# Kernel optimization log

Measured on AMD Instinct MI355X. Metric: run time of the kernel, lower is better.

## Reference

```python
import jax, jax.numpy as jnp
import numpy as np

N, E, F_IN, HEADS, OUT_PER_HEAD = 50000, 1600000, 128, 4, 32
NEG_SLOPE = 0.2  # LeakyReLU slope used by standard GATConv


def setup_inputs() -> dict:
    key = jax.random.key(0)
    ks = jax.random.split(key, 7)
    x = jax.random.normal(ks[0], (N, F_IN), dtype=jnp.float32)
    edge_src = jax.random.randint(ks[1], (E,), 0, N, dtype=jnp.int64)
    edge_dst = jax.random.randint(ks[2], (E,), 0, N, dtype=jnp.int64)
    W = jax.random.normal(ks[3], (F_IN, HEADS * OUT_PER_HEAD), dtype=jnp.float32) / np.float32(np.sqrt(F_IN))
    a_src = jax.random.normal(ks[4], (HEADS, OUT_PER_HEAD), dtype=jnp.float32) * 0.1
    a_dst = jax.random.normal(ks[5], (HEADS, OUT_PER_HEAD), dtype=jnp.float32) * 0.1
    bias = jnp.zeros((HEADS * OUT_PER_HEAD,), dtype=jnp.float32)
    return {"x": x, "W": W, "a_src": a_src, "a_dst": a_dst, "bias": bias,
            "edge_src": edge_src, "edge_dst": edge_dst}


def reference(x, W, a_src, a_dst, bias, edge_src, edge_dst):
    # GATConv with concat=True over a static edge list (the faithful
    # static-shape form of tf.where(adj>0.5) -> gather -> GAT -> scatter).
    n = x.shape[0]
    H, D = a_src.shape
    h = (x @ W).reshape(n, H, D)                      # [N,H,D] projected features
    # per-node attention logits for source / destination roles
    e_s = jnp.einsum('nhd,hd->nh', h, a_src)          # [N,H]
    e_d = jnp.einsum('nhd,hd->nh', h, a_dst)          # [N,H]
    # per-edge logits with LeakyReLU
    e = jax.nn.leaky_relu(e_s[edge_src] + e_d[edge_dst], NEG_SLOPE)  # [E,H]
    # numerically stable softmax over incoming edges of each destination node
    m = jax.ops.segment_max(e, edge_dst, num_segments=n)             # [N,H]
    m = jnp.where(jnp.isfinite(m), m, 0.0)
    alpha = jnp.exp(e - m[edge_dst])                                 # [E,H]
    denom = jax.ops.segment_sum(alpha, edge_dst, num_segments=n)     # [N,H]
    alpha = alpha / jnp.where(denom > 0, denom, 1.0)[edge_dst]
    # weighted aggregation of source features onto destinations
    msgs = alpha[:, :, None] * h[edge_src]                           # [E,H,D]
    out = jax.ops.segment_sum(msgs, edge_dst, num_segments=n)        # [N,H,D]
    return out.reshape(n, H * D) + bias
```

## Files before the change

### kernel.cpp

```cpp
#include <hip/hip_runtime.h>
#include <math.h>

#define NEG_SLOPE 0.2f
#define NB1 256
#define XROW 136
#define BSHIFT 5
#define BNODES 32
#define CAP 2048

typedef __attribute__((ext_vector_type(8))) short short8;
typedef __attribute__((ext_vector_type(4))) float floatx4;

__device__ __forceinline__ unsigned short f2bf(float f) {
    unsigned int u = __float_as_uint(f);
    u += 0x7fffu + ((u >> 16) & 1u);
    return (unsigned short)(u >> 16);
}
__device__ __forceinline__ float bf2f(unsigned short b) {
    return __uint_as_float(((unsigned int)b) << 16);
}
__device__ __forceinline__ float u2fl(unsigned int u) {
    return __uint_as_float(u << 16);
}
__device__ __forceinline__ float u2fh(unsigned int u) {
    return __uint_as_float(u & 0xffff0000u);
}

__device__ __forceinline__ void fma8(float* a, int o, float wt, const uint4& hv) {
    a[o + 0] = fmaf(wt, u2fl(hv.x), a[o + 0]);
    a[o + 1] = fmaf(wt, u2fh(hv.x), a[o + 1]);
    a[o + 2] = fmaf(wt, u2fl(hv.y), a[o + 2]);
    a[o + 3] = fmaf(wt, u2fh(hv.y), a[o + 3]);
    a[o + 4] = fmaf(wt, u2fl(hv.z), a[o + 4]);
    a[o + 5] = fmaf(wt, u2fh(hv.z), a[o + 5]);
    a[o + 6] = fmaf(wt, u2fl(hv.w), a[o + 6]);
    a[o + 7] = fmaf(wt, u2fh(hv.w), a[o + 7]);
}

__global__ __launch_bounds__(256) void prep_w_kernel(
    const float* __restrict__ W, unsigned short* __restrict__ WThi,
    unsigned short* __restrict__ WTlo, int* __restrict__ gcur, int nbuck)
{
    const int idx = blockIdx.x * 256 + threadIdx.x;
    const int j = idx >> 7, k = idx & 127;
    const float w = W[k * 128 + j];
    const unsigned short hi = f2bf(w);
    const unsigned short lo = f2bf(w - bf2f(hi));
    WThi[idx] = hi;
    WTlo[idx] = lo;
    if (idx < nbuck) gcur[idx] = idx * CAP;
}

__global__ __launch_bounds__(256) void mfma_gemm_kernel(
    const float* __restrict__ x, const unsigned short* __restrict__ WThi,
    const unsigned short* __restrict__ WTlo, const float* __restrict__ a_src,
    const float* __restrict__ a_dst, unsigned short* __restrict__ hb,
    float* __restrict__ es, float* __restrict__ ed, int n)
{
    __shared__ unsigned short Xhi[32 * XROW];
    __shared__ unsigned short Xlo[32 * XROW];
    const int t = threadIdx.x;
    const int wv = t >> 6, lane = t & 63;
    const int l16 = lane & 15, quad = lane >> 4;
    const int node_base = blockIdx.x * 32;

    short8 bh[4][2], bl[4][2];
    #pragma unroll
    for (int c = 0; c < 4; ++c) {
        #pragma unroll
        for (int u = 0; u < 2; ++u) {
            const int j = (wv * 2 + u) * 16 + l16;
            const int ko = c * 32 + quad * 8;
            bh[c][u] = *(const short8*)&WThi[j * 128 + ko];
            bl[c][u] = *(const short8*)&WTlo[j * 128 + ko];
        }
    }

    for (int i = t; i < 1024; i += 256) {
        const int nd = i >> 5;
        const int k4 = i & 31;
        float4 xv = make_float4(0.f, 0.f, 0.f, 0.f);
        if (node_base + nd < n)
            xv = ((const float4*)(x + (size_t)(node_base + nd) * 128))[k4];
        const unsigned short h0 = f2bf(xv.x), h1 = f2bf(xv.y),
                             h2 = f2bf(xv.z), h3 = f2bf(xv.w);
        const unsigned short l0 = f2bf(xv.x - bf2f(h0)), l1 = f2bf(xv.y - bf2f(h1)),
                             l2 = f2bf(xv.z - bf2f(h2)), l3 = f2bf(xv.w - bf2f(h3));
        *(ushort4*)&Xhi[nd * XROW + k4 * 4] = make_ushort4(h0, h1, h2, h3);
        *(ushort4*)&Xlo[nd * XROW + k4 * 4] = make_ushort4(l0, l1, l2, l3);
    }
    __syncthreads();

    floatx4 acc[2][2] = {};
    #pragma unroll
    for (int c = 0; c < 4; ++c) {
        const int ko = c * 32 + quad * 8;
        short8 ah[2], al[2];
        #pragma unroll
        for (int r = 0; r < 2; ++r) {
            ah[r] = *(const short8*)&Xhi[(r * 16 + l16) * XROW + ko];
            al[r] = *(const short8*)&Xlo[(r * 16 + l16) * XROW + ko];
        }
        #pragma unroll
        for (int r = 0; r < 2; ++r)
        #pragma unroll
        for (int u = 0; u < 2; ++u) {
            acc[r][u] = __builtin_amdgcn_mfma_f32_16x16x32_bf16(ah[r], bl[c][u], acc[r][u], 0, 0, 0);
            acc[r][u] = __builtin_amdgcn_mfma_f32_16x16x32_bf16(al[r], bh[c][u], acc[r][u], 0, 0, 0);
            acc[r][u] = __builtin_amdgcn_mfma_f32_16x16x32_bf16(ah[r], bh[c][u], acc[r][u], 0, 0, 0);
        }
    }

    float asv[2], adv[2];
    #pragma unroll
    for (int u = 0; u < 2; ++u) {
        const int feat = (wv * 2 + u) * 16 + l16;
        asv[u] = a_src[feat];
        adv[u] = a_dst[feat];
    }
    #pragma unroll
    for (int r = 0; r < 2; ++r) {
        #pragma unroll
        for (int u = 0; u < 2; ++u) {
            const int feat = (wv * 2 + u) * 16 + l16;
            #pragma unroll
            for (int g = 0; g < 4; ++g) {
                const int node = node_base + r * 16 + quad * 4 + g;
                if (node < n)
                    hb[(size_t)node * 128 + feat] = f2bf(acc[r][u][g]);
            }
        }
        #pragma unroll
        for (int g = 0; g < 4; ++g) {
            float ps = acc[r][0][g] * asv[0] + acc[r][1][g] * asv[1];
            float pd = acc[r][0][g] * adv[0] + acc[r][1][g] * adv[1];
            #pragma unroll
            for (int o = 8; o >= 1; o >>= 1) {
                ps += __shfl_xor(ps, o);
                pd += __shfl_xor(pd, o);
            }
            const int node = node_base + r * 16 + quad * 4 + g;
            if (l16 == 0 && node < n) {
                es[node * 4 + wv] = ps;
                ed[node * 4 + wv] = pd;
            }
        }
    }
}

__global__ __launch_bounds__(256) void bucket_scatter(
    const int* __restrict__ src, const int* __restrict__ dst,
    int* __restrict__ gcur, int* __restrict__ ebuf, int e, int nbuck)
{
    __shared__ unsigned int stash[6272];
    __shared__ int cnt[1600];
    __shared__ int cur[1600];
    const int t = threadIdx.x;
    for (int b = t; b < nbuck; b += 256) cnt[b] = 0;
    __syncthreads();
    const int per = (e + NB1 - 1) / NB1;
    const int lo = blockIdx.x * per;
    const int m = min(e, lo + per) - lo;
    for (int j = t; j < m; j += 256) {
        const int d = dst[lo + j];
        const unsigned int v = (unsigned int)src[lo + j]
                             | ((unsigned int)(d & (BNODES - 1)) << 16)
                             | ((unsigned int)(d >> BSHIFT) << 21);
        stash[j] = v;
        atomicAdd(&cnt[d >> BSHIFT], 1);
    }
    __syncthreads();
    for (int b = t; b < nbuck; b += 256) {
        const int c = cnt[b];
        if (c > 0) cur[b] = atomicAdd(&gcur[b], c);
    }
    __syncthreads();
    for (int j = t; j < m; j += 256) {
        const unsigned int v = stash[j];
        const int pos = atomicAdd(&cur[v >> 21], 1);
        ebuf[pos] = (int)(v & 0x1FFFFFu);
    }
}

__global__ __launch_bounds__(256) void sort_agg_kernel(
    const unsigned short* __restrict__ hb, const float* __restrict__ es,
    const float* __restrict__ ed, const float* __restrict__ bias,
    const int* __restrict__ gcur, const int* __restrict__ ebuf,
    float* __restrict__ out, int n)
{
    __shared__ unsigned short esort[CAP];
    __shared__ int hist[BNODES], hexcl[BNODES], cur[BNODES];
    const int b = blockIdx.x;
    const int t = threadIdx.x;
    const int lane = t & 63;
    const int wv = t >> 6;
    const int l8 = lane & 7;
    const int oct = lane >> 3;
    const int f0 = l8 * 16;
    const int hh = l8 >> 1;

    const int start = b * CAP;
    const int end = gcur[b];

    if (t < BNODES) hist[t] = 0;
    __syncthreads();
    for (int i = start + t; i < end; i += 256)
        atomicAdd(&hist[(ebuf[i] >> 16) & (BNODES - 1)], 1);
    __syncthreads();
    if (wv == 0) {
        const int v = (lane < BNODES) ? hist[lane] : 0;
        int incl = v;
        #pragma unroll
        for (int o = 1; o < BNODES; o <<= 1) {
            const int tt = __shfl_up(incl, o);
            if (lane >= o) incl += tt;
        }
        if (lane < BNODES) { hexcl[lane] = incl - v; cur[lane] = incl - v; }
    }
    __syncthreads();
    for (int i = start + t; i < end; i += 256) {
        const int v = ebuf[i];
        const int pos = atomicAdd(&cur[(v >> 16) & (BNODES - 1)], 1);
        esort[pos] = (unsigned short)(v & 0xFFFF);
    }
    __syncthreads();

    for (int j = 0; j < 8; ++j) {
        const int nd = wv * 8 + j;
        const int node = b * BNODES + nd;
        if (node >= n) break;
        const int off = hexcl[nd];
        const int deg = hist[nd];
        const float edh = ed[(size_t)node * 4 + hh];

        float a[16];
        #pragma unroll
        for (int k = 0; k < 16; ++k) a[k] = 0.f;
        float wsum = 0.f;

        for (int c0 = 0; c0 < deg; c0 += 16) {
            const int ci0 = c0 + oct;
            const int ci1 = ci0 + 8;
            const int dm = deg - 1;
            const int s0 = esort[off + min(ci0, dm)];
            const int s1 = esort[off + min(ci1, dm)];
            const float e0 = es[(size_t)s0 * 4 + hh];
            const float e1 = es[(size_t)s1 * 4 + hh];
            const uint4 hA0 = *(const uint4*)&hb[(size_t)s0 * 128 + f0];
            const uint4 hB0 = *(const uint4*)&hb[(size_t)s0 * 128 + f0 + 8];
            const uint4 hA1 = *(const uint4*)&hb[(size_t)s1 * 128 + f0];
            const uint4 hB1 = *(const uint4*)&hb[(size_t)s1 * 128 + f0 + 8];
            float lg0 = e0 + edh; lg0 = lg0 > 0.f ? lg0 : NEG_SLOPE * lg0;
            float lg1 = e1 + edh; lg1 = lg1 > 0.f ? lg1 : NEG_SLOPE * lg1;
            const float w0 = (ci0 < deg) ? __expf(lg0) : 0.f;
            const float w1 = (ci1 < deg) ? __expf(lg1) : 0.f;
            fma8(a, 0, w0, hA0); fma8(a, 8, w0, hB0);
            fma8(a, 0, w1, hA1); fma8(a, 8, w1, hB1);
            wsum += w0 + w1;
        }
        #pragma unroll
        for (int o = 8; o <= 32; o <<= 1) {
            #pragma unroll
            for (int k = 0; k < 16; ++k) a[k] += __shfl_xor(a[k], o);
            wsum += __shfl_xor(wsum, o);
        }
        if (oct == 0) {
            const float inv = 1.f / ((wsum > 0.f) ? wsum : 1.f);
            #pragma unroll
            for (int q = 0; q < 4; ++q) {
                const float4 bq = *(const float4*)(bias + f0 + q * 4);
                float4 o4;
                o4.x = a[q * 4 + 0] * inv + bq.x;
                o4.y = a[q * 4 + 1] * inv + bq.y;
                o4.z = a[q * 4 + 2] * inv + bq.z;
                o4.w = a[q * 4 + 3] * inv + bq.w;
                *(float4*)(out + (size_t)node * 128 + f0 + q * 4) = o4;
            }
        }
    }
}

extern "C" void kernel_launch(void* const* d_in, const int* in_sizes, int n_in,
                              void* d_out, int out_size, void* d_ws, size_t ws_size,
                              hipStream_t stream)
{
    const float* x      = (const float*)d_in[0];
    const float* W      = (const float*)d_in[1];
    const float* a_src  = (const float*)d_in[2];
    const float* a_dst  = (const float*)d_in[3];
    const float* bias   = (const float*)d_in[4];
    const int*   e_src  = (const int*)d_in[5];
    const int*   e_dst  = (const int*)d_in[6];
    float* out = (float*)d_out;

    const int n = in_sizes[0] / 128;
    const int e = in_sizes[5];
    const int nbuck = (n + BNODES - 1) >> BSHIFT;

    char* ws = (char*)d_ws;
    size_t o = 0;
    auto alloc = [&](size_t bytes) { void* p = ws + o; o += (bytes + 255) & ~(size_t)255; return p; };
    unsigned short* hb   = (unsigned short*)alloc((size_t)n * 128 * sizeof(unsigned short));
    unsigned short* WThi = (unsigned short*)alloc(128 * 128 * sizeof(unsigned short));
    unsigned short* WTlo = (unsigned short*)alloc(128 * 128 * sizeof(unsigned short));
    float* es      = (float*)alloc((size_t)n * 4 * sizeof(float));
    float* ed      = (float*)alloc((size_t)n * 4 * sizeof(float));
    int* gcur      = (int*)alloc((size_t)nbuck * sizeof(int));
    int* ebuf      = (int*)alloc((size_t)nbuck * CAP * sizeof(int));
    (void)ws_size; (void)n_in; (void)out_size;

    prep_w_kernel<<<64, 256, 0, stream>>>(W, WThi, WTlo, gcur, nbuck);
    mfma_gemm_kernel<<<(n + 31) / 32, 256, 0, stream>>>(x, WThi, WTlo, a_src, a_dst,
                                                        hb, es, ed, n);
    bucket_scatter<<<NB1, 256, 0, stream>>>(e_src, e_dst, gcur, ebuf, e, nbuck);
    sort_agg_kernel<<<nbuck, 256, 0, stream>>>(hb, es, ed, bias, gcur, ebuf, out, n);
}
```

Measured before the change: 196.7 us.

## Fuse edge bucket scatter into GEMM launch and halve bucket size

Result: no change. 195.7 us (-0.5%).

```diff
diff --git a/kernel.cpp b/kernel.cpp
--- a/kernel.cpp
+++ b/kernel.cpp
@@ -4,9 +4,10 @@
 #define NEG_SLOPE 0.2f
 #define NB1 256
 #define XROW 136
-#define BSHIFT 5
-#define BNODES 32
-#define CAP 2048
+#define BSHIFT 4
+#define BNODES 16
+#define CAP 1024
+#define NBUCK_MAX 3200
 
 typedef __attribute__((ext_vector_type(8))) short short8;
 typedef __attribute__((ext_vector_type(4))) float floatx4;
@@ -51,18 +52,46 @@
     if (idx < nbuck) gcur[idx] = idx * CAP;
 }
 
-__global__ __launch_bounds__(256) void mfma_gemm_kernel(
+__global__ __launch_bounds__(256) void fused_gemm_scatter(
     const float* __restrict__ x, const unsigned short* __restrict__ WThi,
     const unsigned short* __restrict__ WTlo, const float* __restrict__ a_src,
     const float* __restrict__ a_dst, unsigned short* __restrict__ hb,
-    float* __restrict__ es, float* __restrict__ ed, int n)
+    float* __restrict__ es, float* __restrict__ ed, int n,
+    const int* __restrict__ src, const int* __restrict__ dst,
+    int* __restrict__ gcur, int* __restrict__ ebuf, int e, int nbuck)
 {
-    __shared__ unsigned short Xhi[32 * XROW];
-    __shared__ unsigned short Xlo[32 * XROW];
+    __shared__ union {
+        struct { unsigned short Xhi[32 * XROW]; unsigned short Xlo[32 * XROW]; } g;
+        int cnt[NBUCK_MAX];
+    } sm;
+
     const int t = threadIdx.x;
+
+    if (blockIdx.x < NB1) {
+        for (int b = t; b < nbuck; b += 256) sm.cnt[b] = 0;
+        __syncthreads();
+        const int per = (e + NB1 - 1) / NB1;
+        const int lo = blockIdx.x * per;
+        const int m = min(e, lo + per) - lo;
+        for (int j = t; j < m; j += 256)
+            atomicAdd(&sm.cnt[dst[lo + j] >> BSHIFT], 1);
+        __syncthreads();
+        for (int b = t; b < nbuck; b += 256) {
+            const int c = sm.cnt[b];
+            if (c > 0) sm.cnt[b] = atomicAdd(&gcur[b], c);
+        }
+        __syncthreads();
+        for (int j = t; j < m; j += 256) {
+            const int d = dst[lo + j];
+            const int pos = atomicAdd(&sm.cnt[d >> BSHIFT], 1);
+            ebuf[pos] = src[lo + j] | ((d & (BNODES - 1)) << 16);
+        }
+        return;
+    }
+
     const int wv = t >> 6, lane = t & 63;
     const int l16 = lane & 15, quad = lane >> 4;
-    const int node_base = blockIdx.x * 32;
+    const int node_base = (blockIdx.x - NB1) * 32;
 
     short8 bh[4][2], bl[4][2];
     #pragma unroll
@@ -86,8 +115,8 @@
                              h2 = f2bf(xv.z), h3 = f2bf(xv.w);
         const unsigned short l0 = f2bf(xv.x - bf2f(h0)), l1 = f2bf(xv.y - bf2f(h1)),
                              l2 = f2bf(xv.z - bf2f(h2)), l3 = f2bf(xv.w - bf2f(h3));
-        *(ushort4*)&Xhi[nd * XROW + k4 * 4] = make_ushort4(h0, h1, h2, h3);
-        *(ushort4*)&Xlo[nd * XROW + k4 * 4] = make_ushort4(l0, l1, l2, l3);
+        *(ushort4*)&sm.g.Xhi[nd * XROW + k4 * 4] = make_ushort4(h0, h1, h2, h3);
+        *(ushort4*)&sm.g.Xlo[nd * XROW + k4 * 4] = make_ushort4(l0, l1, l2, l3);
     }
     __syncthreads();
 
@@ -98,8 +127,8 @@
         short8 ah[2], al[2];
         #pragma unroll
         for (int r = 0; r < 2; ++r) {
-            ah[r] = *(const short8*)&Xhi[(r * 16 + l16) * XROW + ko];
-            al[r] = *(const short8*)&Xlo[(r * 16 + l16) * XROW + ko];
+            ah[r] = *(const short8*)&sm.g.Xhi[(r * 16 + l16) * XROW + ko];
+            al[r] = *(const short8*)&sm.g.Xlo[(r * 16 + l16) * XROW + ko];
         }
         #pragma unroll
         for (int r = 0; r < 2; ++r)
@@ -145,40 +174,6 @@
                 ed[node * 4 + wv] = pd;
             }
         }
-    }
-}
-
-__global__ __launch_bounds__(256) void bucket_scatter(
-    const int* __restrict__ src, const int* __restrict__ dst,
-    int* __restrict__ gcur, int* __restrict__ ebuf, int e, int nbuck)
-{
-    __shared__ unsigned int stash[6272];
-    __shared__ int cnt[1600];
-    __shared__ int cur[1600];
-    const int t = threadIdx.x;
-    for (int b = t; b < nbuck; b += 256) cnt[b] = 0;
-    __syncthreads();
-    const int per = (e + NB1 - 1) / NB1;
-    const int lo = blockIdx.x * per;
-    const int m = min(e, lo + per) - lo;
-    for (int j = t; j < m; j += 256) {
-        const int d = dst[lo + j];
-        const unsigned int v = (unsigned int)src[lo + j]
-                             | ((unsigned int)(d & (BNODES - 1)) << 16)
-                             | ((unsigned int)(d >> BSHIFT) << 21);
-        stash[j] = v;
-        atomicAdd(&cnt[d >> BSHIFT], 1);
-    }
-    __syncthreads();
-    for (int b = t; b < nbuck; b += 256) {
-        const int c = cnt[b];
-        if (c > 0) cur[b] = atomicAdd(&gcur[b], c);
-    }
-    __syncthreads();
-    for (int j = t; j < m; j += 256) {
-        const unsigned int v = stash[j];
-        const int pos = atomicAdd(&cur[v >> 21], 1);
-        ebuf[pos] = (int)(v & 0x1FFFFFu);
     }
 }
 
@@ -225,8 +220,8 @@
     }
     __syncthreads();
 
-    for (int j = 0; j < 8; ++j) {
-        const int nd = wv * 8 + j;
+    for (int j = 0; j < 4; ++j) {
+        const int nd = wv * 4 + j;
         const int node = b * BNODES + nd;
         if (node >= n) break;
         const int off = hexcl[nd];
@@ -309,9 +304,10 @@
     int* ebuf      = (int*)alloc((size_t)nbuck * CAP * sizeof(int));
     (void)ws_size; (void)n_in; (void)out_size;
 
+    const int ngemm = (n + 31) / 32;
     prep_w_kernel<<<64, 256, 0, stream>>>(W, WThi, WTlo, gcur, nbuck);
-    mfma_gemm_kernel<<<(n + 31) / 32, 256, 0, stream>>>(x, WThi, WTlo, a_src, a_dst,
-                                                        hb, es, ed, n);
-    bucket_scatter<<<NB1, 256, 0, stream>>>(e_src, e_dst, gcur, ebuf, e, nbuck);
+    fused_gemm_scatter<<<NB1 + ngemm, 256, 0, stream>>>(x, WThi, WTlo, a_src, a_dst,
+                                                        hb, es, ed, n,
+                                                        e_src, e_dst, gcur, ebuf, e, nbuck);
     sort_agg_kernel<<<nbuck, 256, 0, stream>>>(hb, es, ed, bias, gcur, ebuf, out, n);
 }
```

## Replace atomic bucket scatter with histogram-scan-scatter and halve bucket size

Applied to the files above, without the earlier changes.

New measurement: 232.3 us. 1.18x slower.

```diff
diff --git a/kernel.cpp b/kernel.cpp
--- a/kernel.cpp
+++ b/kernel.cpp
@@ -2,11 +2,12 @@
 #include <math.h>
 
 #define NEG_SLOPE 0.2f
-#define NB1 256
 #define XROW 136
-#define BSHIFT 5
-#define BNODES 32
-#define CAP 2048
+#define BSHIFT 4
+#define BNODES 16
+#define NBUCK_MAX 3200
+#define CAP 768
+#define NHB 256
 
 typedef __attribute__((ext_vector_type(8))) short short8;
 typedef __attribute__((ext_vector_type(4))) float floatx4;
@@ -37,18 +38,96 @@
     a[o + 7] = fmaf(wt, u2fh(hv.w), a[o + 7]);
 }
 
-__global__ __launch_bounds__(256) void prep_w_kernel(
+__device__ __forceinline__ int eph_of(int e) {
+    return (((e + NHB - 1) / NHB) + 3) & ~3;
+}
+
+__global__ __launch_bounds__(256) void hist_prep_kernel(
     const float* __restrict__ W, unsigned short* __restrict__ WThi,
-    unsigned short* __restrict__ WTlo, int* __restrict__ gcur, int nbuck)
-{
-    const int idx = blockIdx.x * 256 + threadIdx.x;
-    const int j = idx >> 7, k = idx & 127;
-    const float w = W[k * 128 + j];
-    const unsigned short hi = f2bf(w);
-    const unsigned short lo = f2bf(w - bf2f(hi));
-    WThi[idx] = hi;
-    WTlo[idx] = lo;
-    if (idx < nbuck) gcur[idx] = idx * CAP;
+    unsigned short* __restrict__ WTlo, const int* __restrict__ dst,
+    int* __restrict__ C, int e, int nbuck)
+{
+    __shared__ int hist[NBUCK_MAX];
+    const int t = threadIdx.x;
+    const int idx = blockIdx.x * 256 + t;
+    if (idx < 16384) {
+        const int j = idx >> 7, k = idx & 127;
+        const float w = W[k * 128 + j];
+        const unsigned short hi = f2bf(w);
+        WThi[idx] = hi;
+        WTlo[idx] = f2bf(w - bf2f(hi));
+    }
+    for (int b = t; b < nbuck; b += 256) hist[b] = 0;
+    __syncthreads();
+    const int eph = eph_of(e);
+    const int base = blockIdx.x * eph;
+    const int m = min(e - base, eph);
+    if (m > 0) {
+        const int m4 = m >> 2;
+        for (int j = t; j < m4; j += 256) {
+            const int4 d4 = *(const int4*)(dst + base + j * 4);
+            atomicAdd(&hist[d4.x >> BSHIFT], 1);
+            atomicAdd(&hist[d4.y >> BSHIFT], 1);
+            atomicAdd(&hist[d4.z >> BSHIFT], 1);
+            atomicAdd(&hist[d4.w >> BSHIFT], 1);
+        }
+        for (int j = m4 * 4 + t; j < m; j += 256)
+            atomicAdd(&hist[dst[base + j] >> BSHIFT], 1);
+    }
+    __syncthreads();
+    for (int b = t; b < nbuck; b += 256)
+        C[(size_t)blockIdx.x * nbuck + b] = hist[b];
+}
+
+__global__ __launch_bounds__(256) void scan_kernel(
+    int* __restrict__ C, int* __restrict__ btot, int nbuck)
+{
+    const int b = blockIdx.x * 256 + threadIdx.x;
+    if (b >= nbuck) return;
+    int off = 0;
+    #pragma unroll 4
+    for (int k = 0; k < NHB; ++k) {
+        const int v = C[(size_t)k * nbuck + b];
+        C[(size_t)k * nbuck + b] = off;
+        off += v;
+    }
+    btot[b] = off;
+}
+
+__global__ __launch_bounds__(256) void scatter_kernel(
+    const int* __restrict__ src, const int* __restrict__ dst,
+    const int* __restrict__ C, int* __restrict__ ebuf, int e, int nbuck)
+{
+    __shared__ int cur[NBUCK_MAX];
+    const int t = threadIdx.x;
+    for (int b = t; b < nbuck; b += 256)
+        cur[b] = b * CAP + C[(size_t)blockIdx.x * nbuck + b];
+    __syncthreads();
+    const int eph = eph_of(e);
+    const int base = blockIdx.x * eph;
+    const int m = min(e - base, eph);
+    if (m <= 0) return;
+    const int m4 = m >> 2;
+    for (int j = t; j < m4; j += 256) {
+        const int i0 = base + j * 4;
+        const int4 s4 = *(const int4*)(src + i0);
+        const int4 d4 = *(const int4*)(dst + i0);
+        int bk, pos;
+        bk = d4.x >> BSHIFT; pos = atomicAdd(&cur[bk], 1);
+        if (pos < bk * CAP + CAP) ebuf[pos] = s4.x | ((d4.x & 15) << 16);
+        bk = d4.y >> BSHIFT; pos = atomicAdd(&cur[bk], 1);
+        if (pos < bk * CAP + CAP) ebuf[pos] = s4.y | ((d4.y & 15) << 16);
+        bk = d4.z >> BSHIFT; pos = atomicAdd(&cur[bk], 1);
+        if (pos < bk * CAP + CAP) ebuf[pos] = s4.z | ((d4.z & 15) << 16);
+        bk = d4.w >> BSHIFT; pos = atomicAdd(&cur[bk], 1);
+        if (pos < bk * CAP + CAP) ebuf[pos] = s4.w | ((d4.w & 15) << 16);
+    }
+    for (int j = m4 * 4 + t; j < m; j += 256) {
+        const int d = dst[base + j];
+        const int bk = d >> BSHIFT;
+        const int pos = atomicAdd(&cur[bk], 1);
+        if (pos < bk * CAP + CAP) ebuf[pos] = src[base + j] | ((d & 15) << 16);
+    }
 }
 
 __global__ __launch_bounds__(256) void mfma_gemm_kernel(
@@ -148,44 +227,10 @@
     }
 }
 
-__global__ __launch_bounds__(256) void bucket_scatter(
-    const int* __restrict__ src, const int* __restrict__ dst,
-    int* __restrict__ gcur, int* __restrict__ ebuf, int e, int nbuck)
-{
-    __shared__ unsigned int stash[6272];
-    __shared__ int cnt[1600];
-    __shared__ int cur[1600];
-    const int t = threadIdx.x;
-    for (int b = t; b < nbuck; b += 256) cnt[b] = 0;
-    __syncthreads();
-    const int per = (e + NB1 - 1) / NB1;
-    const int lo = blockIdx.x * per;
-    const int m = min(e, lo + per) - lo;
-    for (int j = t; j < m; j += 256) {
-        const int d = dst[lo + j];
-        const unsigned int v = (unsigned int)src[lo + j]
-                             | ((unsigned int)(d & (BNODES - 1)) << 16)
-                             | ((unsigned int)(d >> BSHIFT) << 21);
-        stash[j] = v;
-        atomicAdd(&cnt[d >> BSHIFT], 1);
-    }
-    __syncthreads();
-    for (int b = t; b < nbuck; b += 256) {
-        const int c = cnt[b];
-        if (c > 0) cur[b] = atomicAdd(&gcur[b], c);
-    }
-    __syncthreads();
-    for (int j = t; j < m; j += 256) {
-        const unsigned int v = stash[j];
-        const int pos = atomicAdd(&cur[v >> 21], 1);
-        ebuf[pos] = (int)(v & 0x1FFFFFu);
-    }
-}
-
 __global__ __launch_bounds__(256) void sort_agg_kernel(
     const unsigned short* __restrict__ hb, const float* __restrict__ es,
     const float* __restrict__ ed, const float* __restrict__ bias,
-    const int* __restrict__ gcur, const int* __restrict__ ebuf,
+    const int* __restrict__ btot, const int* __restrict__ ebuf,
     float* __restrict__ out, int n)
 {
     __shared__ unsigned short esort[CAP];
@@ -200,7 +245,7 @@
     const int hh = l8 >> 1;
 
     const int start = b * CAP;
-    const int end = gcur[b];
+    const int end = start + min(btot[b], CAP);
 
     if (t < BNODES) hist[t] = 0;
     __syncthreads();
@@ -221,12 +266,12 @@
     for (int i = start + t; i < end; i += 256) {
         const int v = ebuf[i];
         const int pos = atomicAdd(&cur[(v >> 16) & (BNODES - 1)], 1);
-        esort[pos] = (unsigned short)(v & 0xFFFF);
-    }
-    __syncthreads();
-
-    for (int j = 0; j < 8; ++j) {
-        const int nd = wv * 8 + j;
+        if (pos < CAP) esort[pos] = (unsigned short)(v & 0xFFFF);
+    }
+    __syncthreads();
+
+    for (int j = 0; j < 4; ++j) {
+        const int nd = wv * 4 + j;
         const int node = b * BNODES + nd;
         if (node >= n) break;
         const int off = hexcl[nd];
@@ -242,8 +287,8 @@
             const int ci0 = c0 + oct;
             const int ci1 = ci0 + 8;
             const int dm = deg - 1;
-            const int s0 = esort[off + min(ci0, dm)];
-            const int s1 = esort[off + min(ci1, dm)];
+            const int s0 = esort[min(off + min(ci0, dm), CAP - 1)];
+            const int s1 = esort[min(off + min(ci1, dm), CAP - 1)];
             const float e0 = es[(size_t)s0 * 4 + hh];
             const float e1 = es[(size_t)s1 * 4 + hh];
             const uint4 hA0 = *(const uint4*)&hb[(size_t)s0 * 128 + f0];
@@ -305,13 +350,15 @@
     unsigned short* WTlo = (unsigned short*)alloc(128 * 128 * sizeof(unsigned short));
     float* es      = (float*)alloc((size_t)n * 4 * sizeof(float));
     float* ed      = (float*)alloc((size_t)n * 4 * sizeof(float));
-    int* gcur      = (int*)alloc((size_t)nbuck * sizeof(int));
+    int* C         = (int*)alloc((size_t)NHB * nbuck * sizeof(int));
+    int* btot      = (int*)alloc((size_t)nbuck * sizeof(int));
     int* ebuf      = (int*)alloc((size_t)nbuck * CAP * sizeof(int));
     (void)ws_size; (void)n_in; (void)out_size;
 
-    prep_w_kernel<<<64, 256, 0, stream>>>(W, WThi, WTlo, gcur, nbuck);
+    hist_prep_kernel<<<NHB, 256, 0, stream>>>(W, WThi, WTlo, e_dst, C, e, nbuck);
+    scan_kernel<<<(nbuck + 255) / 256, 256, 0, stream>>>(C, btot, nbuck);
+    scatter_kernel<<<NHB, 256, 0, stream>>>(e_src, e_dst, C, ebuf, e, nbuck);
     mfma_gemm_kernel<<<(n + 31) / 32, 256, 0, stream>>>(x, WThi, WTlo, a_src, a_dst,
                                                         hb, es, ed, n);
-    bucket_scatter<<<NB1, 256, 0, stream>>>(e_src, e_dst, gcur, ebuf, e, nbuck);
-    sort_agg_kernel<<<nbuck, 256, 0, stream>>>(hb, es, ed, bias, gcur, ebuf, out, n);
-}
+    sort_agg_kernel<<<nbuck, 256, 0, stream>>>(hb, es, ed, bias, btot, ebuf, out, n);
+}
```
